# Kernel tuning notes

Hardware: AMD Instinct MI355X
Metric: run time of the kernel (lower is better)

Reference implementation:

```python
import math
import jax, jax.numpy as jnp
import numpy as np

B, T, C, H, DQK, DV = 2, 2048, 1024, 16, 64, 64


def setup_inputs() -> dict:
    key = jax.random.key(0)
    ks = jax.random.split(key, 5)
    x = jax.random.normal(ks[0], (B, T, C), dtype=jnp.float32)
    # randw: randn(*d) / sqrt(d[-1])
    w_q = jax.random.normal(ks[1], (H, DQK, C), dtype=jnp.float32) / math.sqrt(C)
    w_k = jax.random.normal(ks[2], (H, DQK, C), dtype=jnp.float32) / math.sqrt(C)
    w_v = jax.random.normal(ks[3], (H, DV, C), dtype=jnp.float32) / math.sqrt(C)
    w_o = jax.random.normal(ks[4], (DV * H, C), dtype=jnp.float32) / math.sqrt(C)
    return {"x": x, "w_q": w_q, "w_k": w_k, "w_v": w_v, "w_o": w_o}


def reference(x, w_q, w_k, w_v, w_o):
    # Full-sequence causal forward (bs_q.first == 0, nb == T): caches are
    # fully written in one shot, so they reduce to the plain projections.
    n, t, c = x.shape
    q = jnp.einsum('ntc,hdc->nhtd', x, w_q)
    k = jnp.einsum('ntc,hdc->nhtd', x, w_k)
    v = jnp.einsum('ntc,hdc->nhtd', x, w_v)
    scale = 1.0 / math.sqrt(w_q.shape[1])
    a = jnp.einsum('nhtd,nhsd->nhts', q, k) * scale  # [n,h,t,s]
    causal = jnp.arange(t)[:, None] < jnp.arange(t)[None, :]  # True above diag
    a = jnp.where(causal[None, None, :, :], -jnp.inf, a)
    a = jax.nn.softmax(a, axis=3)
    y = jnp.einsum('nhts,nhsd->nthd', a, v).reshape(n, t, -1)  # [n,t,h*dv]
    return y @ w_o  # cache_y, [n,t,c]
```

## Files before the change

### kernel.cpp

```cpp
#include <hip/hip_runtime.h>


typedef short bf16x4 __attribute__((ext_vector_type(4)));
typedef short bf16x8 __attribute__((ext_vector_type(8)));
typedef float f32x4 __attribute__((ext_vector_type(4)));

#define MFMA_BF16 __builtin_amdgcn_mfma_f32_16x16x32_bf16

#define QSCALE 0.18033688011112042f

__device__ __forceinline__ unsigned short f2bf(float f) {
    union { float f; unsigned u; } un; un.f = f;
    unsigned r = un.u + 0x7fffu + ((un.u >> 16) & 1u);
    return (unsigned short)(r >> 16);
}
__device__ __forceinline__ unsigned pk2(float a, float b) {
    return (unsigned)f2bf(a) | ((unsigned)f2bf(b) << 16);
}
__device__ __forceinline__ unsigned pk2t(float a, float b) {
    union { float f; unsigned u; } ua, ub; ua.f = a; ub.f = b;
    return (ua.u >> 16) | (ub.u & 0xffff0000u);
}
__device__ __forceinline__ void gload16(const void* g, void* l) {
    __builtin_amdgcn_global_load_lds(
        (const __attribute__((address_space(1))) unsigned int*)g,
        (__attribute__((address_space(3))) unsigned int*)l, 16, 0, 0);
}

__global__ __launch_bounds__(256) void prep(
    const float* __restrict__ x, const float* __restrict__ wq,
    const float* __restrict__ wk, const float* __restrict__ wv,
    const float* __restrict__ wo,
    unsigned short* __restrict__ x16, unsigned short* __restrict__ wq16,
    unsigned short* __restrict__ wk16, unsigned short* __restrict__ wv16,
    unsigned short* __restrict__ wot)
{
    const int bid = blockIdx.x;
    if (bid < 3584) {
        const float* s; unsigned short* d; int off;
        if (bid < 2048)      { s = x;  d = x16;  off = bid * 2048; }
        else if (bid < 2560) { s = wq; d = wq16; off = (bid - 2048) * 2048; }
        else if (bid < 3072) { s = wk; d = wk16; off = (bid - 2560) * 2048; }
        else                 { s = wv; d = wv16; off = (bid - 3072) * 2048; }
        int i = off + threadIdx.x * 8;
        float4 f0 = *(const float4*)&s[i], f1 = *(const float4*)&s[i + 4];
        uint4 o;
        o.x = pk2(f0.x, f0.y); o.y = pk2(f0.z, f0.w);
        o.z = pk2(f1.x, f1.y); o.w = pk2(f1.z, f1.w);
        *(uint4*)&d[i] = o;
    } else {
        __shared__ unsigned short t[64 * 72];
        const int b2 = bid - 3584;
        const int k0 = (b2 & 15) << 6, n0 = (b2 >> 4) << 6;
        const int r = threadIdx.x >> 2, cg = (threadIdx.x & 3) << 4;
        const float* src = &wo[(k0 + r) * 1024 + n0 + cg];
        #pragma unroll
        for (int j = 0; j < 16; j += 4) {
            float4 f = *(const float4*)&src[j];
            t[(cg + j + 0) * 72 + r] = f2bf(f.x);
            t[(cg + j + 1) * 72 + r] = f2bf(f.y);
            t[(cg + j + 2) * 72 + r] = f2bf(f.z);
            t[(cg + j + 3) * 72 + r] = f2bf(f.w);
        }
        __syncthreads();
        unsigned short* dst = &wot[(n0 + r) * 1024 + k0 + cg];
        unsigned short* tr = &t[r * 72 + cg];
        unsigned v[16];
        #pragma unroll
        for (int j = 0; j < 16; ++j) v[j] = tr[j];
        uint4 o0, o1;
        o0.x = v[0] | (v[1] << 16);   o0.y = v[2] | (v[3] << 16);
        o0.z = v[4] | (v[5] << 16);   o0.w = v[6] | (v[7] << 16);
        o1.x = v[8] | (v[9] << 16);   o1.y = v[10] | (v[11] << 16);
        o1.z = v[12] | (v[13] << 16); o1.w = v[14] | (v[15] << 16);
        *(uint4*)&dst[0] = o0;
        *(uint4*)&dst[8] = o1;
    }
}

__device__ __forceinline__ void gemm_body(
    const unsigned short* __restrict__ A, const unsigned short* __restrict__ Bm,
    void* __restrict__ C, int m0, int n0, int mode, int ldc, float sc)
{
    __shared__ unsigned short sa[2][128 * 32];
    __shared__ unsigned short sb[2][128 * 32];
    const int tid = threadIdx.x, wave = tid >> 6, lane = tid & 63;
    const int l15 = lane & 15, l4 = lane >> 4;
    const int wm = (wave >> 1) << 6, wn = (wave & 1) << 6;

    const int r16 = lane >> 2;
    const int gcol = (((lane & 3) ^ ((r16 >> 1) & 3)) << 3);
    const int rcol = (l4 ^ ((l15 >> 1) & 3)) << 3;
    const unsigned short* Ag0 = &A[(size_t)(m0 + wave * 16 + r16) * 1024 + gcol];
    const unsigned short* Ag1 = Ag0 + (size_t)64 * 1024;
    const unsigned short* Bg0 = &Bm[(size_t)(n0 + wave * 16 + r16) * 1024 + gcol];
    const unsigned short* Bg1 = Bg0 + (size_t)64 * 1024;
    const int lb0 = (wave * 16) * 32;
    const int lb1 = (64 + wave * 16) * 32;

    gload16(Ag0, &sa[0][lb0]);
    gload16(Ag1, &sa[0][lb1]);
    gload16(Bg0, &sb[0][lb0]);
    gload16(Bg1, &sb[0][lb1]);
    __syncthreads();

    f32x4 acc[4][4] = {};

    #pragma unroll
    for (int kk = 0; kk < 32; ++kk) {
        const int cur = kk & 1;
        if (kk < 31) {
            const int off = (kk + 1) * 32;
            const int nxt = 1 - cur;
            gload16(Ag0 + off, &sa[nxt][lb0]);
            gload16(Ag1 + off, &sa[nxt][lb1]);
            gload16(Bg0 + off, &sb[nxt][lb0]);
            gload16(Bg1 + off, &sb[nxt][lb1]);
        }
        bf16x8 af[4], bf4[4];
        #pragma unroll
        for (int i = 0; i < 4; ++i)
            af[i] = *(const bf16x8*)&sa[cur][(wm + i * 16 + l15) * 32 + rcol];
        #pragma unroll
        for (int j = 0; j < 4; ++j)
            bf4[j] = *(const bf16x8*)&sb[cur][(wn + j * 16 + l15) * 32 + rcol];
        #pragma unroll
        for (int i = 0; i < 4; ++i)
            #pragma unroll
            for (int j = 0; j < 4; ++j)
                acc[i][j] = MFMA_BF16(af[i], bf4[j], acc[i][j], 0, 0, 0);
        __syncthreads();
    }

    #pragma unroll
    for (int i = 0; i < 4; ++i)
        #pragma unroll
        for (int j = 0; j < 4; ++j)
            #pragma unroll
            for (int r = 0; r < 4; ++r) {
                int row = m0 + wm + i * 16 + l4 * 4 + r;
                int col = n0 + wn + j * 16 + l15;
                float val = acc[i][j][r];
                if (mode == 0) {
                    int nb = row >> 11, t = row & 2047;
                    int hh = col >> 6, dd = col & 63;
                    ((unsigned short*)C)[(((nb << 4) + hh) * 2048 + t) * 64 + dd] =
                        f2bf(val * sc);
                } else if (mode == 1) {
                    ((float*)C)[(size_t)row * ldc + col] = val;
                } else {
                    int s = col & 31;
                    int cp = (col & ~31) | (((s >> 2) & 3) << 3)
                                         | (((s >> 4) & 1) << 2) | (s & 3);
                    ((unsigned short*)C)[(size_t)row * ldc + cp] = f2bf(val);
                }
            }
}

__global__ __launch_bounds__(256) void proj(
    const unsigned short* __restrict__ x16,
    const unsigned short* __restrict__ wq16,
    const unsigned short* __restrict__ wk16,
    const unsigned short* __restrict__ wv16,
    unsigned short* __restrict__ qbuf,
    unsigned short* __restrict__ kbuf,
    unsigned short* __restrict__ vtb)
{
    const int bid = blockIdx.x;
    if (bid < 512) {
        int m0 = (bid & 31) << 7;
        int n0g = (bid >> 5) << 7;
        if (n0g < 1024)
            gemm_body(x16, wq16, qbuf, m0, n0g, 0, 0, QSCALE);
        else
            gemm_body(x16, wk16, kbuf, m0, n0g - 1024, 0, 0, 1.0f);
    } else {
        int v = bid - 512;
        gemm_body(wv16, x16, vtb, (v & 7) << 7, (v >> 3) << 7, 2, 4096, 1.0f);
    }
}

__global__ __launch_bounds__(256) void outp(
    const unsigned short* __restrict__ ybuf,
    const unsigned short* __restrict__ wot,
    float* __restrict__ out)
{
    const int bid = blockIdx.x;
    gemm_body(ybuf, wot, out, (bid & 31) << 7, (bid >> 5) << 7, 1, 1024, 1.0f);
}

__global__ __launch_bounds__(256) void attn(
    const unsigned short* __restrict__ q,
    const unsigned short* __restrict__ k,
    const unsigned short* __restrict__ vt,
    unsigned short* __restrict__ y)
{
    __shared__ unsigned short sk[2][64 * 64];
    __shared__ unsigned short sv[2][64 * 64];
    const int tid = threadIdx.x, wave = tid >> 6, lane = tid & 63;
    const int l15 = lane & 15, l4 = lane >> 4;
    const int bid = blockIdx.x;
    const int qtt = 15 - (bid >> 5);
    const int bh = bid & 31;
    const int nb = bh >> 4, hh = bh & 15;
    const int q0 = qtt << 7;
    const size_t base = (size_t)bh << 17;

    const int lrow = lane >> 3;
    const int gch = ((lane & 7) ^ lrow) << 3;
    const int row0 = wave * 8 + lrow, row1 = 32 + wave * 8 + lrow;
    const unsigned short* kg0 = &k[base + (size_t)row0 * 64 + gch];
    const unsigned short* kg1 = &k[base + (size_t)row1 * 64 + gch];
    const unsigned short* vg0 = &vt[(size_t)((hh << 6) + row0) * 4096 + (nb << 11) + gch];
    const unsigned short* vg1 = &vt[(size_t)((hh << 6) + row1) * 4096 + (nb << 11) + gch];
    const int lbk0 = (wave * 8) * 64, lbk1 = (32 + wave * 8) * 64;

    bf16x8 qf[2][2];
    #pragma unroll
    for (int g = 0; g < 2; ++g)
        #pragma unroll
        for (int ks = 0; ks < 2; ++ks)
            qf[g][ks] = *(const bf16x8*)
                &q[base + (size_t)(q0 + (g << 6) + wave * 16 + l15) * 64 + ks * 32 + l4 * 8];

    float l_sum[2] = {0.f, 0.f};
    f32x4 acc[2][4] = {};

    const int nst = 2 * qtt + 2;

    const int rch0 = ((0 + l4) ^ (l15 & 7)) << 3;
    const int rch1 = ((4 + l4) ^ (l15 & 7)) << 3;

    gload16(kg0, &sk[0][lbk0]);
    gload16(kg1, &sk[0][lbk1]);
    gload16(vg0, &sv[0][lbk0]);
    gload16(vg1, &sv[0][lbk1]);
    __syncthreads();

    auto step = [&](const int cur, const int st, const bool more) {
        if (more) {
            const int nxt = cur ^ 1;
            const int s1e = (st + 1) << 6;
            gload16(kg0 + ((size_t)s1e << 6), &sk[nxt][lbk0]);
            gload16(kg1 + ((size_t)s1e << 6), &sk[nxt][lbk1]);
            gload16(vg0 + s1e, &sv[nxt][lbk0]);
            gload16(vg1 + s1e, &sv[nxt][lbk1]);
        }

        f32x4 s_acc[2][4] = {};
        #pragma unroll
        for (int ns = 0; ns < 4; ++ns) {
            bf16x8 kf0 = *(const bf16x8*)&sk[cur][(ns * 16 + l15) * 64 + rch0];
            bf16x8 kf1 = *(const bf16x8*)&sk[cur][(ns * 16 + l15) * 64 + rch1];
            s_acc[0][ns] = MFMA_BF16(kf0, qf[0][0], s_acc[0][ns], 0, 0, 0);
            s_acc[0][ns] = MFMA_BF16(kf1, qf[0][1], s_acc[0][ns], 0, 0, 0);
            s_acc[1][ns] = MFMA_BF16(kf0, qf[1][0], s_acc[1][ns], 0, 0, 0);
            s_acc[1][ns] = MFMA_BF16(kf1, qf[1][1], s_acc[1][ns], 0, 0, 0);
        }

        if (st >= nst - 2) {
            const int sb = st << 6;
            #pragma unroll
            for (int g = 0; g < 2; ++g) {
                const int qlg = q0 + (g << 6) + wave * 16 + l15;
                #pragma unroll
                for (int ns = 0; ns < 4; ++ns)
                    #pragma unroll
                    for (int r = 0; r < 4; ++r)
                        if (sb + ns * 16 + l4 * 4 + r > qlg) s_acc[g][ns][r] = -1e30f;
            }
        }

        float pe[2][4][4];
        #pragma unroll
        for (int g = 0; g < 2; ++g)
            #pragma unroll
            for (int ns = 0; ns < 4; ++ns) {
                #pragma unroll
                for (int r = 0; r < 4; ++r) pe[g][ns][r] = exp2f(s_acc[g][ns][r]);
                l_sum[g] += (pe[g][ns][0] + pe[g][ns][1]) + (pe[g][ns][2] + pe[g][ns][3]);
            }

        #pragma unroll
        for (int ks = 0; ks < 2; ++ks) {
            bf16x8 pf0, pf1;
            {
                uint4 pw;
                pw.x = pk2t(pe[0][2 * ks][0], pe[0][2 * ks][1]);
                pw.y = pk2t(pe[0][2 * ks][2], pe[0][2 * ks][3]);
                pw.z = pk2t(pe[0][2 * ks + 1][0], pe[0][2 * ks + 1][1]);
                pw.w = pk2t(pe[0][2 * ks + 1][2], pe[0][2 * ks + 1][3]);
                pf0 = *(bf16x8*)&pw;
            }
            {
                uint4 pw;
                pw.x = pk2t(pe[1][2 * ks][0], pe[1][2 * ks][1]);
                pw.y = pk2t(pe[1][2 * ks][2], pe[1][2 * ks][3]);
                pw.z = pk2t(pe[1][2 * ks + 1][0], pe[1][2 * ks + 1][1]);
                pw.w = pk2t(pe[1][2 * ks + 1][2], pe[1][2 * ks + 1][3]);
                pf1 = *(bf16x8*)&pw;
            }
            const int rch = ks ? rch1 : rch0;
            #pragma unroll
            for (int ds = 0; ds < 4; ++ds) {
                bf16x8 vf = *(const bf16x8*)&sv[cur][(ds * 16 + l15) * 64 + rch];
                acc[0][ds] = MFMA_BF16(vf, pf0, acc[0][ds], 0, 0, 0);
                acc[1][ds] = MFMA_BF16(vf, pf1, acc[1][ds], 0, 0, 0);
            }
        }
        __syncthreads();
    };

    int st = 0;
    for (; st + 2 <= nst; st += 2) {
        step(0, st, true);
        step(1, st + 1, (st + 2) < nst);
    }
    if (st < nst) step(0, st, false);

    #pragma unroll
    for (int g = 0; g < 2; ++g) {
        float ls = l_sum[g];
        ls += __shfl_xor(ls, 16);
        ls += __shfl_xor(ls, 32);
        const float rl = __builtin_amdgcn_rcpf(ls);

        const size_t rowbase =
            ((size_t)((nb << 11) + q0 + (g << 6) + wave * 16 + l15) << 10) + (hh << 6) + l4 * 4;
        #pragma unroll
        for (int ds = 0; ds < 4; ++ds) {
            uint2 o;
            o.x = pk2(acc[g][ds][0] * rl, acc[g][ds][1] * rl);
            o.y = pk2(acc[g][ds][2] * rl, acc[g][ds][3] * rl);
            *(uint2*)&y[rowbase + ds * 16] = o;
        }
    }
}

extern "C" void kernel_launch(void* const* d_in, const int* in_sizes, int n_in,
                              void* d_out, int out_size, void* d_ws, size_t ws_size,
                              hipStream_t stream) {
    const float* x  = (const float*)d_in[0];
    const float* wq = (const float*)d_in[1];
    const float* wk = (const float*)d_in[2];
    const float* wv = (const float*)d_in[3];
    const float* wo = (const float*)d_in[4];
    float* out = (float*)d_out;

    const size_t M1 = 1u << 20;
    unsigned short* x16  = (unsigned short*)d_ws;
    unsigned short* wq16 = x16 + 4 * M1;
    unsigned short* wk16 = wq16 + M1;
    unsigned short* wv16 = wk16 + M1;
    unsigned short* wot  = wv16 + M1;
    unsigned short* qbuf = wot + M1;
    unsigned short* kbuf = qbuf + 4 * M1;
    unsigned short* vtb  = kbuf + 4 * M1;
    unsigned short* ybuf = vtb + 4 * M1;

    dim3 blk(256);
    prep<<<3840, blk, 0, stream>>>(x, wq, wk, wv, wo, x16, wq16, wk16, wv16, wot);
    proj<<<768, blk, 0, stream>>>(x16, wq16, wk16, wv16, qbuf, kbuf, vtb);
    attn<<<512, blk, 0, stream>>>(qbuf, kbuf, vtb, ybuf);
    outp<<<256, blk, 0, stream>>>(ybuf, wot, out);
}
```

Baseline: 176.6 us.

## Use 128x64 output-projection tiles and reorder attention query tiles

The output projection gets its own GEMM kernel with 128x64 tiles, doubling the grid from 256 to 512 blocks so more CUs stay busy on the 4096x1024 output. It uses a double-buffered LDS pipeline with async global-to-LDS loads. The attention block-to-query-tile mapping also changes: the first half of blocks runs the longest causal tiles in descending order and the second half runs ascending, to improve load balance. Smaller tiles mean less data reuse per block, and the new ordering may not balance better than the old one.

```diff
diff --git a/kernel.cpp b/kernel.cpp
--- a/kernel.cpp
+++ b/kernel.cpp
@@ -185,8 +185,66 @@
     const unsigned short* __restrict__ wot,
     float* __restrict__ out)
 {
+    __shared__ unsigned short sa[2][128 * 32];
+    __shared__ unsigned short sb[2][64 * 32];
+    const int tid = threadIdx.x, wave = tid >> 6, lane = tid & 63;
+    const int l15 = lane & 15, l4 = lane >> 4;
     const int bid = blockIdx.x;
-    gemm_body(ybuf, wot, out, (bid & 31) << 7, (bid >> 5) << 7, 1, 1024, 1.0f);
+    const int m0 = (bid & 31) << 7;
+    const int n0 = (bid >> 5) << 6;
+    const int wm = (wave >> 1) << 6, wn = (wave & 1) << 5;
+
+    const int r16 = lane >> 2;
+    const int gcol = (((lane & 3) ^ ((r16 >> 1) & 3)) << 3);
+    const int rcol = (l4 ^ ((l15 >> 1) & 3)) << 3;
+    const unsigned short* Ag0 = &ybuf[(size_t)(m0 + wave * 16 + r16) * 1024 + gcol];
+    const unsigned short* Ag1 = Ag0 + (size_t)64 * 1024;
+    const unsigned short* Bg0 = &wot[(size_t)(n0 + wave * 16 + r16) * 1024 + gcol];
+    const int lba0 = (wave * 16) * 32, lba1 = (64 + wave * 16) * 32;
+    const int lbb = (wave * 16) * 32;
+
+    gload16(Ag0, &sa[0][lba0]);
+    gload16(Ag1, &sa[0][lba1]);
+    gload16(Bg0, &sb[0][lbb]);
+    __syncthreads();
+
+    f32x4 acc[4][2] = {};
+
+    #pragma unroll
+    for (int kk = 0; kk < 32; ++kk) {
+        const int cur = kk & 1;
+        if (kk < 31) {
+            const int off = (kk + 1) * 32;
+            const int nxt = 1 - cur;
+            gload16(Ag0 + off, &sa[nxt][lba0]);
+            gload16(Ag1 + off, &sa[nxt][lba1]);
+            gload16(Bg0 + off, &sb[nxt][lbb]);
+        }
+        bf16x8 af[4], bf2[2];
+        #pragma unroll
+        for (int i = 0; i < 4; ++i)
+            af[i] = *(const bf16x8*)&sa[cur][(wm + i * 16 + l15) * 32 + rcol];
+        #pragma unroll
+        for (int j = 0; j < 2; ++j)
+            bf2[j] = *(const bf16x8*)&sb[cur][(wn + j * 16 + l15) * 32 + rcol];
+        #pragma unroll
+        for (int i = 0; i < 4; ++i)
+            #pragma unroll
+            for (int j = 0; j < 2; ++j)
+                acc[i][j] = MFMA_BF16(af[i], bf2[j], acc[i][j], 0, 0, 0);
+        __syncthreads();
+    }
+
+    #pragma unroll
+    for (int i = 0; i < 4; ++i)
+        #pragma unroll
+        for (int j = 0; j < 2; ++j)
+            #pragma unroll
+            for (int r = 0; r < 4; ++r) {
+                int row = m0 + wm + i * 16 + l4 * 4 + r;
+                int col = n0 + wn + j * 16 + l15;
+                out[(size_t)row * 1024 + col] = acc[i][j][r];
+            }
 }
 
 __global__ __launch_bounds__(256) void attn(
@@ -200,7 +258,7 @@
     const int tid = threadIdx.x, wave = tid >> 6, lane = tid & 63;
     const int l15 = lane & 15, l4 = lane >> 4;
     const int bid = blockIdx.x;
-    const int qtt = 15 - (bid >> 5);
+    const int qtt = (bid < 256) ? (15 - (bid >> 5)) : ((bid >> 5) - 8);
     const int bh = bid & 31;
     const int nb = bh >> 4, hh = bh & 15;
     const int q0 = qtt << 7;
@@ -362,5 +420,5 @@
     prep<<<3840, blk, 0, stream>>>(x, wq, wk, wv, wo, x16, wq16, wk16, wv16, wot);
     proj<<<768, blk, 0, stream>>>(x16, wq16, wk16, wv16, qbuf, kbuf, vtb);
     attn<<<512, blk, 0, stream>>>(qbuf, kbuf, vtb, ybuf);
-    outp<<<256, blk, 0, stream>>>(ybuf, wot, out);
-}
+    outp<<<512, blk, 0, stream>>>(ybuf, wot, out);
+}
```

New measurement: 180.3 us. 2.1% more time.

## Triple-buffer K/V loads in attention with vmcnt-based waits and reorder tiles

Applied to the files above, without the earlier changes.

Moves the attention kernel's K/V staging from double to triple buffering, issuing loads two steps ahead. Each step now ends with an explicit s_waitcnt on the vector-memory counter plus a raw barrier, replacing the full __syncthreads drain. The block-to-q-tile mapping is changed so the second half of blocks runs tiles in ascending order, evening out causal work per wave of blocks. It also swaps the bf16 truncation pack for a single v_perm, at the cost of more LDS per block, which may reduce occupancy.

```diff
diff --git a/kernel.cpp b/kernel.cpp
--- a/kernel.cpp
+++ b/kernel.cpp
@@ -19,7 +19,7 @@
 }
 __device__ __forceinline__ unsigned pk2t(float a, float b) {
     union { float f; unsigned u; } ua, ub; ua.f = a; ub.f = b;
-    return (ua.u >> 16) | (ub.u & 0xffff0000u);
+    return __builtin_amdgcn_perm(ub.u, ua.u, 0x07060302u);
 }
 __device__ __forceinline__ void gload16(const void* g, void* l) {
     __builtin_amdgcn_global_load_lds(
@@ -195,12 +195,12 @@
     const unsigned short* __restrict__ vt,
     unsigned short* __restrict__ y)
 {
-    __shared__ unsigned short sk[2][64 * 64];
-    __shared__ unsigned short sv[2][64 * 64];
+    __shared__ unsigned short sk[3][64 * 64];
+    __shared__ unsigned short sv[3][64 * 64];
     const int tid = threadIdx.x, wave = tid >> 6, lane = tid & 63;
     const int l15 = lane & 15, l4 = lane >> 4;
     const int bid = blockIdx.x;
-    const int qtt = 15 - (bid >> 5);
+    const int qtt = (bid < 256) ? (15 - (bid >> 5)) : ((bid >> 5) - 8);
     const int bh = bid & 31;
     const int nb = bh >> 4, hh = bh & 15;
     const int q0 = qtt << 7;
@@ -222,6 +222,7 @@
         for (int ks = 0; ks < 2; ++ks)
             qf[g][ks] = *(const bf16x8*)
                 &q[base + (size_t)(q0 + (g << 6) + wave * 16 + l15) * 64 + ks * 32 + l4 * 8];
+    asm volatile("s_waitcnt vmcnt(0)" ::: "memory");
 
     float l_sum[2] = {0.f, 0.f};
     f32x4 acc[2][4] = {};
@@ -231,21 +232,24 @@
     const int rch0 = ((0 + l4) ^ (l15 & 7)) << 3;
     const int rch1 = ((4 + l4) ^ (l15 & 7)) << 3;
 
-    gload16(kg0, &sk[0][lbk0]);
-    gload16(kg1, &sk[0][lbk1]);
-    gload16(vg0, &sv[0][lbk0]);
-    gload16(vg1, &sv[0][lbk1]);
-    __syncthreads();
-
-    auto step = [&](const int cur, const int st, const bool more) {
-        if (more) {
-            const int nxt = cur ^ 1;
-            const int s1e = (st + 1) << 6;
-            gload16(kg0 + ((size_t)s1e << 6), &sk[nxt][lbk0]);
-            gload16(kg1 + ((size_t)s1e << 6), &sk[nxt][lbk1]);
-            gload16(vg0 + s1e, &sv[nxt][lbk0]);
-            gload16(vg1 + s1e, &sv[nxt][lbk1]);
-        }
+    auto stage = [&](const int sbuf, const int st) {
+        const size_t ko = (size_t)st << 12;
+        const int vo = st << 6;
+        gload16(kg0 + ko, &sk[sbuf][lbk0]);
+        gload16(kg1 + ko, &sk[sbuf][lbk1]);
+        gload16(vg0 + vo, &sv[sbuf][lbk0]);
+        gload16(vg1 + vo, &sv[sbuf][lbk1]);
+    };
+
+    stage(0, 0);
+    stage(1, 1);
+    asm volatile("s_waitcnt vmcnt(4)" ::: "memory");
+    __builtin_amdgcn_s_barrier();
+    asm volatile("" ::: "memory");
+
+    auto step = [&](const int cur, const int nxt, const int st) {
+        const bool issue = (st + 2) < nst;
+        if (issue) stage(nxt, st + 2);
 
         f32x4 s_acc[2][4] = {};
         #pragma unroll
@@ -308,15 +312,23 @@
                 acc[1][ds] = MFMA_BF16(vf, pf1, acc[1][ds], 0, 0, 0);
             }
         }
-        __syncthreads();
+
+        if (issue) asm volatile("s_waitcnt vmcnt(4)" ::: "memory");
+        else       asm volatile("s_waitcnt vmcnt(0)" ::: "memory");
+        __builtin_amdgcn_s_barrier();
+        asm volatile("" ::: "memory");
     };
 
     int st = 0;
-    for (; st + 2 <= nst; st += 2) {
-        step(0, st, true);
-        step(1, st + 1, (st + 2) < nst);
-    }
-    if (st < nst) step(0, st, false);
+    for (; st + 3 <= nst; st += 3) {
+        step(0, 2, st);
+        step(1, 0, st + 1);
+        step(2, 1, st + 2);
+    }
+    if (st < nst) {
+        step(0, 2, st);
+        if (st + 1 < nst) step(1, 0, st + 1);
+    }
 
     #pragma unroll
     for (int g = 0; g < 2; ++g) {
```

Result: no change. 175.7 us (-0.5%).

## Split attention KV loop across two wave groups with LDS merge of partials

Applied to the files above, without the earlier changes.

The attention kernel now uses 512 threads per block. Two groups of four waves each process alternate 64-key tiles from a shared double-buffered pair of K/V tiles, then merge their partial accumulators and row sums through LDS before normalising and writing. This halves the serial KV-loop length per block and raises the number of waves in flight, at the cost of a final LDS reduction, more LDS per block and a changed block-to-tile order (second half of blocks ascending). The bf16 truncating pack also switches to a single byte-permute instruction.

```diff
diff --git a/kernel.cpp b/kernel.cpp
--- a/kernel.cpp
+++ b/kernel.cpp
@@ -19,7 +19,7 @@
 }
 __device__ __forceinline__ unsigned pk2t(float a, float b) {
     union { float f; unsigned u; } ua, ub; ua.f = a; ub.f = b;
-    return (ua.u >> 16) | (ub.u & 0xffff0000u);
+    return __builtin_amdgcn_perm(ub.u, ua.u, 0x07060302u);
 }
 __device__ __forceinline__ void gload16(const void* g, void* l) {
     __builtin_amdgcn_global_load_lds(
@@ -189,18 +189,19 @@
     gemm_body(ybuf, wot, out, (bid & 31) << 7, (bid >> 5) << 7, 1, 1024, 1.0f);
 }
 
-__global__ __launch_bounds__(256) void attn(
+__global__ __launch_bounds__(512, 4) void attn(
     const unsigned short* __restrict__ q,
     const unsigned short* __restrict__ k,
     const unsigned short* __restrict__ vt,
     unsigned short* __restrict__ y)
 {
-    __shared__ unsigned short sk[2][64 * 64];
-    __shared__ unsigned short sv[2][64 * 64];
+    __shared__ unsigned short sk[2][2][64 * 64];
+    __shared__ unsigned short sv[2][2][64 * 64];
     const int tid = threadIdx.x, wave = tid >> 6, lane = tid & 63;
+    const int ws = wave & 3, wk2 = wave >> 2;
     const int l15 = lane & 15, l4 = lane >> 4;
     const int bid = blockIdx.x;
-    const int qtt = 15 - (bid >> 5);
+    const int qtt = (bid < 256) ? (15 - (bid >> 5)) : ((bid >> 5) - 8);
     const int bh = bid & 31;
     const int nb = bh >> 4, hh = bh & 15;
     const int q0 = qtt << 7;
@@ -208,12 +209,10 @@
 
     const int lrow = lane >> 3;
     const int gch = ((lane & 7) ^ lrow) << 3;
-    const int row0 = wave * 8 + lrow, row1 = 32 + wave * 8 + lrow;
-    const unsigned short* kg0 = &k[base + (size_t)row0 * 64 + gch];
-    const unsigned short* kg1 = &k[base + (size_t)row1 * 64 + gch];
-    const unsigned short* vg0 = &vt[(size_t)((hh << 6) + row0) * 4096 + (nb << 11) + gch];
-    const unsigned short* vg1 = &vt[(size_t)((hh << 6) + row1) * 4096 + (nb << 11) + gch];
-    const int lbk0 = (wave * 8) * 64, lbk1 = (32 + wave * 8) * 64;
+    const int row = wave * 8 + lrow;
+    const unsigned short* kg = &k[base + (size_t)row * 64 + gch];
+    const unsigned short* vg = &vt[(size_t)((hh << 6) + row) * 4096 + (nb << 11) + gch];
+    const int lb = (wave * 8) * 64;
 
     bf16x8 qf[2][2];
     #pragma unroll
@@ -221,48 +220,48 @@
         #pragma unroll
         for (int ks = 0; ks < 2; ++ks)
             qf[g][ks] = *(const bf16x8*)
-                &q[base + (size_t)(q0 + (g << 6) + wave * 16 + l15) * 64 + ks * 32 + l4 * 8];
+                &q[base + (size_t)(q0 + (g << 6) + ws * 16 + l15) * 64 + ks * 32 + l4 * 8];
 
     float l_sum[2] = {0.f, 0.f};
     f32x4 acc[2][4] = {};
 
-    const int nst = 2 * qtt + 2;
+    const int nsup = qtt + 1;
 
     const int rch0 = ((0 + l4) ^ (l15 & 7)) << 3;
     const int rch1 = ((4 + l4) ^ (l15 & 7)) << 3;
 
-    gload16(kg0, &sk[0][lbk0]);
-    gload16(kg1, &sk[0][lbk1]);
-    gload16(vg0, &sv[0][lbk0]);
-    gload16(vg1, &sv[0][lbk1]);
+    auto stage_pair = [&](const int sbuf, const int p) {
+        gload16(kg + ((size_t)p << 13),        &sk[sbuf][0][lb]);
+        gload16(kg + ((size_t)p << 13) + 4096, &sk[sbuf][1][lb]);
+        gload16(vg + (p << 7),      &sv[sbuf][0][lb]);
+        gload16(vg + (p << 7) + 64, &sv[sbuf][1][lb]);
+    };
+
+    stage_pair(0, 0);
     __syncthreads();
 
-    auto step = [&](const int cur, const int st, const bool more) {
-        if (more) {
-            const int nxt = cur ^ 1;
-            const int s1e = (st + 1) << 6;
-            gload16(kg0 + ((size_t)s1e << 6), &sk[nxt][lbk0]);
-            gload16(kg1 + ((size_t)s1e << 6), &sk[nxt][lbk1]);
-            gload16(vg0 + s1e, &sv[nxt][lbk0]);
-            gload16(vg1 + s1e, &sv[nxt][lbk1]);
-        }
+    auto sstep = [&](const int cur, const int p) {
+        if (p + 1 < nsup) stage_pair(cur ^ 1, p + 1);
+        const int st = 2 * p + wk2;
+        const unsigned short* skc = &sk[cur][wk2][0];
+        const unsigned short* svc = &sv[cur][wk2][0];
 
         f32x4 s_acc[2][4] = {};
         #pragma unroll
         for (int ns = 0; ns < 4; ++ns) {
-            bf16x8 kf0 = *(const bf16x8*)&sk[cur][(ns * 16 + l15) * 64 + rch0];
-            bf16x8 kf1 = *(const bf16x8*)&sk[cur][(ns * 16 + l15) * 64 + rch1];
+            bf16x8 kf0 = *(const bf16x8*)&skc[(ns * 16 + l15) * 64 + rch0];
+            bf16x8 kf1 = *(const bf16x8*)&skc[(ns * 16 + l15) * 64 + rch1];
             s_acc[0][ns] = MFMA_BF16(kf0, qf[0][0], s_acc[0][ns], 0, 0, 0);
             s_acc[0][ns] = MFMA_BF16(kf1, qf[0][1], s_acc[0][ns], 0, 0, 0);
             s_acc[1][ns] = MFMA_BF16(kf0, qf[1][0], s_acc[1][ns], 0, 0, 0);
             s_acc[1][ns] = MFMA_BF16(kf1, qf[1][1], s_acc[1][ns], 0, 0, 0);
         }
 
-        if (st >= nst - 2) {
+        if (p == nsup - 1) {
             const int sb = st << 6;
             #pragma unroll
             for (int g = 0; g < 2; ++g) {
-                const int qlg = q0 + (g << 6) + wave * 16 + l15;
+                const int qlg = q0 + (g << 6) + ws * 16 + l15;
                 #pragma unroll
                 for (int ns = 0; ns < 4; ++ns)
                     #pragma unroll
@@ -303,7 +302,7 @@
             const int rch = ks ? rch1 : rch0;
             #pragma unroll
             for (int ds = 0; ds < 4; ++ds) {
-                bf16x8 vf = *(const bf16x8*)&sv[cur][(ds * 16 + l15) * 64 + rch];
+                bf16x8 vf = *(const bf16x8*)&svc[(ds * 16 + l15) * 64 + rch];
                 acc[0][ds] = MFMA_BF16(vf, pf0, acc[0][ds], 0, 0, 0);
                 acc[1][ds] = MFMA_BF16(vf, pf1, acc[1][ds], 0, 0, 0);
             }
@@ -311,28 +310,56 @@
         __syncthreads();
     };
 
-    int st = 0;
-    for (; st + 2 <= nst; st += 2) {
-        step(0, st, true);
-        step(1, st + 1, (st + 2) < nst);
-    }
-    if (st < nst) step(0, st, false);
-
-    #pragma unroll
-    for (int g = 0; g < 2; ++g) {
-        float ls = l_sum[g];
-        ls += __shfl_xor(ls, 16);
-        ls += __shfl_xor(ls, 32);
-        const float rl = __builtin_amdgcn_rcpf(ls);
-
-        const size_t rowbase =
-            ((size_t)((nb << 11) + q0 + (g << 6) + wave * 16 + l15) << 10) + (hh << 6) + l4 * 4;
-        #pragma unroll
-        for (int ds = 0; ds < 4; ++ds) {
-            uint2 o;
-            o.x = pk2(acc[g][ds][0] * rl, acc[g][ds][1] * rl);
-            o.y = pk2(acc[g][ds][2] * rl, acc[g][ds][3] * rl);
-            *(uint2*)&y[rowbase + ds * 16] = o;
+    int p = 0;
+    for (; p + 2 <= nsup; p += 2) {
+        sstep(0, p);
+        sstep(1, p + 1);
+    }
+    if (p < nsup) sstep(0, p);
+
+    float* mrg = (float*)&sk[0][0][0];
+    float* lsr = (float*)&sv[0][0][0];
+    const int mb = ((ws << 6) + lane) << 5;
+    if (wk2 == 1) {
+        #pragma unroll
+        for (int g = 0; g < 2; ++g)
+            #pragma unroll
+            for (int ds = 0; ds < 4; ++ds) {
+                const int c = g * 4 + ds;
+                *(f32x4*)&mrg[mb + ((c ^ (lane & 7)) << 2)] = acc[g][ds];
+            }
+        lsr[(((ws << 6) + lane) << 1) + 0] = l_sum[0];
+        lsr[(((ws << 6) + lane) << 1) + 1] = l_sum[1];
+    }
+    __syncthreads();
+    if (wk2 == 0) {
+        #pragma unroll
+        for (int g = 0; g < 2; ++g)
+            #pragma unroll
+            for (int ds = 0; ds < 4; ++ds) {
+                const int c = g * 4 + ds;
+                f32x4 o = *(const f32x4*)&mrg[mb + ((c ^ (lane & 7)) << 2)];
+                acc[g][ds] += o;
+            }
+        l_sum[0] += lsr[(((ws << 6) + lane) << 1) + 0];
+        l_sum[1] += lsr[(((ws << 6) + lane) << 1) + 1];
+
+        #pragma unroll
+        for (int g = 0; g < 2; ++g) {
+            float ls = l_sum[g];
+            ls += __shfl_xor(ls, 16);
+            ls += __shfl_xor(ls, 32);
+            const float rl = __builtin_amdgcn_rcpf(ls);
+
+            const size_t rowbase =
+                ((size_t)((nb << 11) + q0 + (g << 6) + ws * 16 + l15) << 10) + (hh << 6) + l4 * 4;
+            #pragma unroll
+            for (int ds = 0; ds < 4; ++ds) {
+                uint2 o;
+                o.x = pk2(acc[g][ds][0] * rl, acc[g][ds][1] * rl);
+                o.y = pk2(acc[g][ds][2] * rl, acc[g][ds][3] * rl);
+                *(uint2*)&y[rowbase + ds * 16] = o;
+            }
         }
     }
 }
@@ -361,6 +388,6 @@
     dim3 blk(256);
     prep<<<3840, blk, 0, stream>>>(x, wq, wk, wv, wo, x16, wq16, wk16, wv16, wot);
     proj<<<768, blk, 0, stream>>>(x16, wq16, wk16, wv16, qbuf, kbuf, vtb);
-    attn<<<512, blk, 0, stream>>>(qbuf, kbuf, vtb, ybuf);
+    attn<<<512, dim3(512), 0, stream>>>(qbuf, kbuf, vtb, ybuf);
     outp<<<256, blk, 0, stream>>>(ybuf, wot, out);
 }
```

Result: no change. 173.7 us (-1.7%).
